# Kernel optimization log

Measured on AMD Instinct MI355X. Metric: run time of the kernel, lower is better.

Reference implementation:

```python
import jax, jax.numpy as jnp
import numpy as np
import math

# ---------- real Clebsch-Gordan coupling tables (computed once, tiny) ----------
def _cg(j1, m1, j2, m2, j3, m3):
    if m1 + m2 != m3 or j3 < abs(j1 - j2) or j3 > j1 + j2:
        return 0.0
    f = math.factorial
    pre = ((2 * j3 + 1) * f(j3 + j1 - j2) * f(j3 - j1 + j2) * f(j1 + j2 - j3) / f(j1 + j2 + j3 + 1)) ** 0.5
    pre *= (f(j3 + m3) * f(j3 - m3) * f(j1 - m1) * f(j1 + m1) * f(j2 - m2) * f(j2 + m2)) ** 0.5
    s = 0.0
    for k in range(0, j1 + j2 - j3 + 1):
        d = (k, j1 + j2 - j3 - k, j1 - m1 - k, j2 + m2 - k, j3 - j2 + m1 + k, j3 - j1 - m2 + k)
        if min(d) < 0:
            continue
        den = 1
        for t in d:
            den *= f(t)
        s += (-1) ** k / den
    return pre * s

def _Q(l):  # complex->real spherical-harmonic change of basis
    Q = np.zeros((2 * l + 1, 2 * l + 1), dtype=complex)
    Q[l, l] = 1.0
    s = 2 ** -0.5
    for m in range(1, l + 1):
        Q[l + m, l + m] = (-1) ** m * s
        Q[l + m, l - m] = s
        Q[l - m, l + m] = -1j * (-1) ** m * s
        Q[l - m, l - m] = 1j * s
    return Q

def _K(l1, l2, l3):  # real coupling tensor [2l3+1, 2l1+1, 2l2+1]
    C = np.zeros((2 * l3 + 1, 2 * l1 + 1, 2 * l2 + 1), dtype=complex)
    for M3 in range(-l3, l3 + 1):
        for M1 in range(-l1, l1 + 1):
            for M2 in range(-l2, l2 + 1):
                C[M3 + l3, M1 + l1, M2 + l2] = _cg(l1, M1, l2, M2, l3, M3)
    K = np.einsum('cC,aA,bB,CAB->cab', _Q(l3).conj(), _Q(l1), _Q(l2), C)
    K = K.imag if np.abs(K.imag).max() > np.abs(K.real).max() else K.real
    return np.asarray(K, dtype=np.float32)

# the 9 'uvu' instructions (in_l, edge_l, out_l) with multiplicities (weight_numel=144)
_PATHS = [(0, 0, 0), (0, 2, 2), (1, 0, 1), (1, 2, 1), (1, 2, 2), (2, 0, 2), (2, 2, 0), (2, 2, 1), (2, 2, 2)]
_KT = [jnp.asarray(_K(*p)) for p in _PATHS]
_MULS = [32, 32, 16, 16, 16, 8, 8, 8, 8]
_SPLITS = np.cumsum(_MULS)[:-1].tolist()
NEI = 8
EPS = 1e-5

def _sh(u):  # component-normalized real SH of unit vectors, l=0..2 (m order -l..l, l=1 -> y,z,x)
    x, y, z = u[:, 0], u[:, 1], u[:, 2]
    sh0 = jnp.ones_like(x)[:, None]
    sh1 = np.float32(3 ** 0.5) * jnp.stack([y, z, x], -1)
    s15 = np.float32(15 ** 0.5)
    s5 = np.float32(5 ** 0.5)
    sh2 = jnp.stack([s15 * x * y, s15 * y * z, 0.5 * s5 * (3 * z * z - 1.0), s15 * x * z, 0.5 * s15 * (x * x - y * y)], -1)
    return sh0, sh1, sh2

def _path(xs, sh, wp, Kt):  # xs [E,u,2l1+1], sh [E,2l2+1], Kt [2l3+1,2l1+1,2l2+1] -> [E,u,2l3+1]
    return jnp.einsum('eui,ej,oij->euo', xs, sh, Kt) * wp[None, :, None]

def _layer(x0, x1, x2, pos, src, dst, w, W0, W1, W2, bw0, bb0, bw1, bw2, N):
    ev = pos[dst] - pos[src]
    u = ev / (jnp.linalg.norm(ev, axis=1, keepdims=True) + 1e-12)
    sh0, sh1, sh2 = _sh(u)
    s0 = x0[src][:, :, None]  # [E,32,1]
    s1 = x1[src]              # [E,16,3]
    s2 = x2[src]              # [E,8,5]
    ws = jnp.split(w, _SPLITS)
    p1 = _path(s0, sh0, ws[0], _KT[0])
    p2 = _path(s0, sh2, ws[1], _KT[1])
    p3 = _path(s1, sh0, ws[2], _KT[2])
    p4 = _path(s1, sh2, ws[3], _KT[3])
    p5 = _path(s1, sh2, ws[4], _KT[4])
    p6 = _path(s2, sh0, ws[5], _KT[5])
    p7 = _path(s2, sh2, ws[6], _KT[6])
    p8 = _path(s2, sh2, ws[7], _KT[7])
    p9 = _path(s2, sh2, ws[8], _KT[8])
    m0 = jnp.concatenate([p1, p7], 1)          # [E,40,1]
    m1 = jnp.concatenate([p3, p4, p8], 1)      # [E,40,3]
    m2 = jnp.concatenate([p2, p5, p6, p9], 1)  # [E,64,5]
    a0 = jax.ops.segment_sum(m0, dst, num_segments=N)
    a1 = jax.ops.segment_sum(m1, dst, num_segments=N)
    a2 = jax.ops.segment_sum(m2, dst, num_segments=N)
    y0 = (a0[:, :, 0] @ W0) * np.float32(1.0 / 40 ** 0.5)
    y1 = jnp.einsum('num,uv->nvm', a1, W1) * np.float32(1.0 / 40 ** 0.5)
    y2 = jnp.einsum('num,uv->nvm', a2, W2) * np.float32(1.0 / 64 ** 0.5)
    # equivariant batchnorm (training stats): scalars -> standard BN, l>0 -> norm BN
    f = y0 - y0.mean(0)
    y0 = f / jnp.sqrt((f * f).mean(0) + EPS) * bw0 + bb0
    y1 = y1 / jnp.sqrt((y1 * y1).mean(axis=(0, 2)) + EPS)[None, :, None] * bw1[None, :, None]
    y2 = y2 / jnp.sqrt((y2 * y2).mean(axis=(0, 2)) + EPS)[None, :, None] * bw2[None, :, None]
    return y0, y1, y2

def _forward(positions, W_emb, tp_w, lin_W0, lin_W1, lin_W2, bn_w0, bn_b0, bn_w1, bn_w2, Wf1, Wf2, bf2, Wf3, bf3):
    B, P, _ = positions.shape
    N = B * P
    pos = positions.reshape(N, 3)
    # kNN graph from dense cdist + topk (indices are not differentiated)
    pg = jax.lax.stop_gradient(pos)
    sq = jnp.sum(pg * pg, 1)
    d2 = sq[:, None] + sq[None, :] - 2.0 * (pg @ pg.T)
    _, idx = jax.lax.top_k(-d2, NEI + 1)  # smallest distances; col 0 is self
    src = jnp.repeat(jnp.arange(N), NEI)
    dst = idx[:, 1:].reshape(-1)
    x0 = jnp.ones((N, 1), jnp.float32) @ W_emb  # embedding: only 0e->0e path exists
    x1 = jnp.zeros((N, 16, 3), jnp.float32)
    x2 = jnp.zeros((N, 8, 5), jnp.float32)
    for l in range(3):
        y0, y1, y2 = _layer(x0, x1, x2, pos, src, dst, tp_w[l], lin_W0[l], lin_W1[l], lin_W2[l],
                            bn_w0[l], bn_b0[l], bn_w1[l], bn_w2[l], N)
        x0 = jax.nn.relu(y0) + x0
        x1 = jax.nn.relu(y1) + x1
        x2 = jax.nn.relu(y2) + x2
    h = jax.nn.relu((x0 @ Wf1) * np.float32(1.0 / 32 ** 0.5))  # scalar part -> 32x0e
    h = jax.nn.relu(h @ Wf2 + bf2)
    out = (h @ Wf3 + bf3).reshape(B, P, 2)
    return out

def setup_inputs() -> dict:
    key = jax.random.key(0)
    ks = jax.random.split(key, 16)
    B, P = 4, 2048
    return {
        'positions': jax.random.normal(ks[0], (B, P, 3), jnp.float32) * 3.0,
        'W_emb': jax.random.normal(ks[1], (1, 32), jnp.float32),
        'tp_w': jax.random.normal(ks[2], (3, 144), jnp.float32),
        'lin_W0': jax.random.normal(ks[3], (3, 40, 32), jnp.float32),
        'lin_W1': jax.random.normal(ks[4], (3, 40, 16), jnp.float32),
        'lin_W2': jax.random.normal(ks[5], (3, 64, 8), jnp.float32),
        'bn_w0': 1.0 + 0.05 * jax.random.normal(ks[6], (3, 32), jnp.float32),
        'bn_b0': jnp.zeros((3, 32), jnp.float32),
        'bn_w1': 1.0 + 0.05 * jax.random.normal(ks[7], (3, 16), jnp.float32),
        'bn_w2': 1.0 + 0.05 * jax.random.normal(ks[8], (3, 8), jnp.float32),
        'Wf1': jax.random.normal(ks[9], (32, 32), jnp.float32),
        'Wf2': jax.random.normal(ks[10], (32, 16), jnp.float32) * 0.2,
        'bf2': jax.random.normal(ks[11], (16,), jnp.float32) * 0.1,
        'Wf3': jax.random.normal(ks[12], (16, 2), jnp.float32) * 0.2,
        'bf3': jax.random.normal(ks[13], (2,), jnp.float32) * 0.1,
    }

def reference(positions, W_emb, tp_w, lin_W0, lin_W1, lin_W2, bn_w0, bn_b0, bn_w1, bn_w2, Wf1, Wf2, bf2, Wf3, bf3):
    return _forward(positions, W_emb, tp_w, lin_W0, lin_W1, lin_W2, bn_w0, bn_b0, bn_w1, bn_w2, Wf1, Wf2, bf2, Wf3, bf3)
```

## Files before the change

kernel.cpp:

```cpp
#include <hip/hip_runtime.h>
#include <math.h>

#define NN 8192
#define REV_CAP 48
#define KNN_CAP 384
#define PF 12

static const size_t OFF_K     = 0;
static const size_t OFF_CNT   = 512;
static const size_t OFF_REV   = 8704;
static const size_t OFF_STATS = 401920;
static const size_t OFF_XF    = 406528;
static const size_t OFF_YF    = 1389568;
static const size_t WS_FLOATS = 2372608;

__device__ double dfact(int n){ double r=1.0; for(int i=2;i<=n;++i) r*=(double)i; return r; }

__device__ double dcg(int j1,int m1,int j2,int m2,int j3,int m3){
  if (m1+m2!=m3) return 0.0;
  if (j3 < abs(j1-j2) || j3 > j1+j2) return 0.0;
  double pre = sqrt((double)(2*j3+1)*dfact(j3+j1-j2)*dfact(j3-j1+j2)*dfact(j1+j2-j3)/dfact(j1+j2+j3+1));
  pre *= sqrt(dfact(j3+m3)*dfact(j3-m3)*dfact(j1-m1)*dfact(j1+m1)*dfact(j2-m2)*dfact(j2+m2));
  double s=0.0;
  for(int k=0;k<=j1+j2-j3;++k){
    int d1=j1+j2-j3-k, d2=j1-m1-k, d3=j2+m2-k, d4=j3-j2+m1+k, d5=j3-j1-m2+k;
    if(d1<0||d2<0||d3<0||d4<0||d5<0) continue;
    double den = dfact(k)*dfact(d1)*dfact(d2)*dfact(d3)*dfact(d4)*dfact(d5);
    s += ((k&1)? -1.0: 1.0)/den;
  }
  return pre*s;
}

__device__ int qrow(int l,int r,int* col,double* re,double* im){
  const double s = 0.70710678118654752440;
  if (r==l){ col[0]=l; re[0]=1.0; im[0]=0.0; return 1; }
  if (r>l){ int m=r-l;
    col[0]=l+m; re[0]=((m&1)?-s:s); im[0]=0.0;
    col[1]=l-m; re[1]=s;            im[1]=0.0;
  } else { int m=l-r;
    col[0]=l+m; re[0]=0.0; im[0]=((m&1)? s : -s);
    col[1]=l-m; re[1]=0.0; im[1]=s;
  }
  return 2;
}

__global__ __launch_bounds__(256) void k_setup(const float* __restrict__ pos,
        const float* __restrict__ W_emb, float* __restrict__ Kbuf,
        float* __restrict__ xf,
        float* __restrict__ xs, float* __restrict__ ys, float* __restrict__ zs,
        float* __restrict__ qs,
        int* __restrict__ cnt){
  int idx = blockIdx.x*256 + threadIdx.x;
  if (idx < 983040) { const int c = idx%120; xf[idx] = (c<32)? W_emb[c] : 0.f; return; }
  idx -= 983040;
  if (idx < 8192) {
    const float x=pos[3*idx], y=pos[3*idx+1], z=pos[3*idx+2];
    xs[idx]=x; ys[idx]=y; zs[idx]=z; qs[idx]=0.5f*(x*x+y*y+z*z);
    return;
  }
  idx -= 8192;
  if (idx < 8192) { cnt[idx]=0; return; }
  idx -= 8192;
  if (idx >= 405) return;

  const int tid = idx;
  const int sizes[9]={1,25,9,45,75,25,25,75,125};
  const int l1s[9]={0,0,1,1,1,2,2,2,2};
  const int l2s[9]={0,2,0,2,2,0,2,2,2};
  const int l3s[9]={0,2,1,1,2,2,0,1,2};
  int p=0, rem=tid;
  for(p=0;p<9;++p){ if(rem < sizes[p]) break; rem -= sizes[p]; }
  const int l1=l1s[p], l2=l2s[p], l3=l3s[p];
  const int n1=2*l1+1, n2=2*l2+1;
  const int c = rem/(n1*n2); const int r2 = rem%(n1*n2); const int a=r2/n2; const int b=r2%n2;

  int c3[2],c1[2],c2[2]; double re3[2],im3[2],re1[2],im1[2],re2[2],im2[2];
  const int nc3 = qrow(l3,c,c3,re3,im3);
  const int nc1 = qrow(l1,a,c1,re1,im1);
  const int nc2 = qrow(l2,b,c2,re2,im2);

  double accRe=0, accIm=0;
  for(int i3=0;i3<nc3;++i3){
    const double q3re=re3[i3], q3im=-im3[i3];
    for(int i1=0;i1<nc1;++i1){
      const double pre_re = q3re*re1[i1] - q3im*im1[i1];
      const double pre_im = q3re*im1[i1] + q3im*re1[i1];
      for(int i2=0;i2<nc2;++i2){
        const double cgv = dcg(l1, c1[i1]-l1, l2, c2[i2]-l2, l3, c3[i3]-l3);
        if (cgv==0.0) continue;
        accRe += (pre_re*re2[i2] - pre_im*im2[i2])*cgv;
        accIm += (pre_re*im2[i2] + pre_im*re2[i2])*cgv;
      }
    }
  }
  const bool useImag = ((l1+l2+l3)&1)!=0;
  Kbuf[tid] = (float)(useImag? accIm : accRe);
}

__device__ __forceinline__ unsigned fkey(float f){
  const unsigned b = __float_as_uint(f);
  return (b & 0x80000000u) ? ~b : (b | 0x80000000u);
}

__global__ __launch_bounds__(256) void k_knn8(const float* __restrict__ xs,
                                              const float* __restrict__ ys,
                                              const float* __restrict__ zs,
                                              const float* __restrict__ qs,
                                              int* __restrict__ cnt, int* __restrict__ rev){
  const int lane = threadIdx.x & 63;
  const int w    = threadIdx.x >> 6;
  const int node = blockIdx.x*4 + w;
  __shared__ float sdist[4][KNN_CAP];
  __shared__ int   sidx[4][KNN_CAP];
  __shared__ int   scount[4];
  if (threadIdx.x < 4) scount[threadIdx.x]=0;
  __syncthreads();

  const float px = xs[node], py = ys[node], pz = zs[node];

  float m1 = INFINITY, m2 = INFINITY;
  for(int c=0;c<4;++c){
    const int base = (c*64 + lane)*4;
    const float4 fx = *(const float4*)(xs + base);
    const float4 fy = *(const float4*)(ys + base);
    const float4 fz = *(const float4*)(zs + base);
    const float4 fq = *(const float4*)(qs + base);
    float ss[4];
    ss[0] = fmaf(-px,fx.x, fmaf(-py,fy.x, fmaf(-pz,fz.x, fq.x)));
    ss[1] = fmaf(-px,fx.y, fmaf(-py,fy.y, fmaf(-pz,fz.y, fq.y)));
    ss[2] = fmaf(-px,fx.z, fmaf(-py,fy.z, fmaf(-pz,fz.z, fq.z)));
    ss[3] = fmaf(-px,fx.w, fmaf(-py,fy.w, fmaf(-pz,fz.w, fq.w)));
    #pragma unroll
    for(int q=0;q<4;++q){
      const float hi = fmaxf(m1, ss[q]);
      m1 = fminf(m1, ss[q]);
      m2 = fminf(m2, hi);
    }
  }
  {
    const unsigned kk1 = fkey(m1), kk2 = fkey(m2);
    unsigned P = 0u; int need = 9;
    #pragma unroll 1
    for(int bit=31; bit>=0; --bit){
      const unsigned pref = P >> bit;
      const int c0 = __popcll(__ballot((kk1>>bit)==pref)) + __popcll(__ballot((kk2>>bit)==pref));
      if (need > c0){ need -= c0; P |= (1u<<bit); }
    }
    m1 = __uint_as_float((P & 0x80000000u) ? (P & 0x7fffffffu) : ~P);
  }
  const float T = m1;

  for(int c=0;c<32;++c){
    const int base = (c*64 + lane)*4;
    const float4 fx = *(const float4*)(xs + base);
    const float4 fy = *(const float4*)(ys + base);
    const float4 fz = *(const float4*)(zs + base);
    const float4 fq = *(const float4*)(qs + base);
    float ss[4];
    ss[0] = fmaf(-px,fx.x, fmaf(-py,fy.x, fmaf(-pz,fz.x, fq.x)));
    ss[1] = fmaf(-px,fx.y, fmaf(-py,fy.y, fmaf(-pz,fz.y, fq.y)));
    ss[2] = fmaf(-px,fx.z, fmaf(-py,fy.z, fmaf(-pz,fz.z, fq.z)));
    ss[3] = fmaf(-px,fx.w, fmaf(-py,fy.w, fmaf(-pz,fz.w, fq.w)));
    #pragma unroll
    for(int q=0;q<4;++q){
      if (ss[q] <= T){
        int pos = atomicAdd(&scount[w],1);
        if (pos < KNN_CAP){ sdist[w][pos]=ss[q]; sidx[w][pos]=base+q; }
      }
    }
  }
  __syncthreads();

  int m = scount[w]; if (m > KNN_CAP) m = KNN_CAP;
  unsigned ku[KNN_CAP/64]; int il[KNN_CAP/64];
  #pragma unroll
  for(int k=0;k<KNN_CAP/64;++k){
    const int j = lane + 64*k;
    if (j < m){ ku[k]=fkey(sdist[w][j]); il[k]=sidx[w][j]; }
    else      { ku[k]=0xffffffffu;       il[k]=0x7fffffff; }
  }
  unsigned P = 0u; int need = 9;
  #pragma unroll 1
  for(int bit=31; bit>=0; --bit){
    const unsigned pref = P >> bit;
    int c0 = 0;
    #pragma unroll
    for(int k=0;k<KNN_CAP/64;++k) c0 += __popcll(__ballot((ku[k]>>bit)==pref));
    if (need > c0){ need -= c0; P |= (1u<<bit); }
  }
  int c_eq = 0;
  #pragma unroll
  for(int k=0;k<KNN_CAP/64;++k) c_eq += __popcll(__ballot(ku[k]==P));
  bool tsel[KNN_CAP/64];
  #pragma unroll
  for(int k=0;k<KNN_CAP/64;++k) tsel[k] = (ku[k]==P);
  if (c_eq > need){
    #pragma unroll
    for(int k=0;k<KNN_CAP/64;++k) tsel[k]=false;
    for(int r=0;r<need;++r){
      int mid = 0x7fffffff;
      #pragma unroll
      for(int k=0;k<KNN_CAP/64;++k) if (ku[k]==P && !tsel[k] && il[k]<mid) mid = il[k];
      #pragma unroll
      for(int s=32;s>0;s>>=1){ const int om = __shfl_xor(mid,s,64); mid = (om<mid)? om : mid; }
      #pragma unroll
      for(int k=0;k<KNN_CAP/64;++k) if (ku[k]==P && il[k]==mid) tsel[k]=true;
    }
  }
  #pragma unroll
  for(int k=0;k<KNN_CAP/64;++k){
    const bool take = (ku[k] < P) || tsel[k];
    const int ix = il[k];
    if (take && ix != node){
      int cpos = atomicAdd(&cnt[ix],1);
      if (cpos < REV_CAP) rev[ix*REV_CAP + cpos] = node;
    }
  }
}

__global__ __launch_bounds__(256) void k_msg(
  const float* __restrict__ pos,
  const int* __restrict__ cnt, const int* __restrict__ rev,
  const float* __restrict__ Kbuf,
  const float* __restrict__ xf,
  const float* __restrict__ tpw,
  const float* __restrict__ W0, const float* __restrict__ W1, const float* __restrict__ W2,
  float* __restrict__ yf)
{
  const int t = threadIdx.x;
  const int w = t >> 6;
  const int lane = t & 63;
  const int n = blockIdx.x*4 + w;

  __shared__ float KL[405];
  __shared__ float TW[144];
  __shared__ float momP[4][120];
  __shared__ float momS[4][600];
  __shared__ float aS[4][480];
  __shared__ int   eIdx[4][REV_CAP];
  __shared__ float eSh[4][5][REV_CAP];
  for(int q=t;q<405;q+=256) KL[q]=Kbuf[q];
  for(int q=t;q<144;q+=256) TW[q]=tpw[q];

  const int deg0 = cnt[n];
  const int deg = (deg0<REV_CAP)? deg0 : REV_CAP;
  const float pnx=pos[3*n], pny=pos[3*n+1], pnz=pos[3*n+2];
  const float s15 = 3.8729833462f, s5c = 2.2360679775f;
  if (lane < deg){
    const int i = rev[n*REV_CAP+lane];
    eIdx[w][lane] = i;
    const float ex = pnx - pos[3*i], ey = pny - pos[3*i+1], ez = pnz - pos[3*i+2];
    const float rn = sqrtf(ex*ex+ey*ey+ez*ez) + 1e-12f;
    const float ux=ex/rn, uy=ey/rn, uz=ez/rn;
    eSh[w][0][lane]=s15*ux*uy;
    eSh[w][1][lane]=s15*uy*uz;
    eSh[w][2][lane]=0.5f*s5c*(3.f*uz*uz-1.f);
    eSh[w][3][lane]=s15*ux*uz;
    eSh[w][4][lane]=0.5f*s15*(ux*ux-uy*uy);
  }
  __syncthreads();

  const int c0 = lane*2;
  float mp0=0.f, mp1=0.f;
  float ms0[5], ms1[5];
  #pragma unroll
  for(int j=0;j<5;++j){ ms0[j]=0.f; ms1[j]=0.f; }

  int idxr[PF];
  #pragma unroll
  for(int k=0;k<PF;++k) idxr[k] = (k<deg)? eIdx[w][k] : 0;
  float2 fr[PF];
  if (lane<60){
    #pragma unroll
    for(int k=0;k<PF;++k) fr[k] = *(const float2*)(xf + (size_t)idxr[k]*120 + c0);
  }
  #pragma unroll
  for(int k=0;k<PF;++k){
    if (k<deg){
      const float sh0=eSh[w][0][k], sh1=eSh[w][1][k], sh2=eSh[w][2][k];
      const float sh3=eSh[w][3][k], sh4=eSh[w][4][k];
      if (lane<60){
        const float2 f = fr[k];
        mp0 += f.x; mp1 += f.y;
        ms0[0]+=f.x*sh0; ms0[1]+=f.x*sh1; ms0[2]+=f.x*sh2; ms0[3]+=f.x*sh3; ms0[4]+=f.x*sh4;
        ms1[0]+=f.y*sh0; ms1[1]+=f.y*sh1; ms1[2]+=f.y*sh2; ms1[3]+=f.y*sh3; ms1[4]+=f.y*sh4;
      }
    }
  }
  for(int e=PF;e<deg;++e){
    const int i = eIdx[w][e];
    const float sh0=eSh[w][0][e], sh1=eSh[w][1][e], sh2=eSh[w][2][e];
    const float sh3=eSh[w][3][e], sh4=eSh[w][4][e];
    if (lane<60){
      const float2 f = *(const float2*)(xf + (size_t)i*120 + c0);
      mp0 += f.x; mp1 += f.y;
      ms0[0]+=f.x*sh0; ms0[1]+=f.x*sh1; ms0[2]+=f.x*sh2; ms0[3]+=f.x*sh3; ms0[4]+=f.x*sh4;
      ms1[0]+=f.y*sh0; ms1[1]+=f.y*sh1; ms1[2]+=f.y*sh2; ms1[3]+=f.y*sh3; ms1[4]+=f.y*sh4;
    }
  }
  if (lane<60){
    momP[w][c0]=mp0; momP[w][c0+1]=mp1;
    #pragma unroll
    for(int j=0;j<5;++j){ momS[w][c0*5+j]=ms0[j]; momS[w][(c0+1)*5+j]=ms1[j]; }
  }
  __syncthreads();

  float acc[14];
  #pragma unroll
  for(int k=0;k<14;++k) acc[k]=0.f;

  if (lane<32){
    const int u=lane;
    const float rw0=TW[u], rw1=TW[32+u];
    acc[0] = rw0 * KL[0] * momP[w][u];
    float m0s[5];
    #pragma unroll
    for(int j=0;j<5;++j) m0s[j]=momS[w][u*5+j];
    #pragma unroll
    for(int o=0;o<5;++o){ float g=0.f;
      #pragma unroll
      for(int j=0;j<5;++j) g += KL[1+o*5+j]*m0s[j];
      acc[1+o] = rw1*g; }
  } else if (lane<48){
    const int u=lane-32;
    const float rw0=TW[64+u], rw1=TW[80+u], rw2=TW[96+u];
    float m1p[3], m1s[3][5];
    #pragma unroll
    for(int i=0;i<3;++i){
      m1p[i]=momP[w][32+u*3+i];
      #pragma unroll
      for(int j=0;j<5;++j) m1s[i][j]=momS[w][(32+u*3+i)*5+j];
    }
    #pragma unroll
    for(int o=0;o<3;++o){ float g=0.f;
      #pragma unroll
      for(int i=0;i<3;++i) g += KL[26+o*3+i]*m1p[i];
      acc[o]=rw0*g; }
    #pragma unroll
    for(int o=0;o<3;++o){ float g=0.f;
      #pragma unroll
      for(int i=0;i<3;++i)
        #pragma unroll
        for(int j=0;j<5;++j) g += KL[35+(o*3+i)*5+j]*m1s[i][j];
      acc[3+o]=rw1*g; }
    #pragma unroll
    for(int o=0;o<5;++o){ float g=0.f;
      #pragma unroll
      for(int i=0;i<3;++i)
        #pragma unroll
        for(int j=0;j<5;++j) g += KL[80+(o*3+i)*5+j]*m1s[i][j];
      acc[6+o]=rw2*g; }
  } else if (lane<56){
    const int u=lane-48;
    const float rw0=TW[112+u], rw1=TW[120+u], rw2=TW[128+u], rw3=TW[136+u];
    float m2p[5], m2s[5][5];
    #pragma unroll
    for(int i=0;i<5;++i){
      m2p[i]=momP[w][80+u*5+i];
      #pragma unroll
      for(int j=0;j<5;++j) m2s[i][j]=momS[w][(80+u*5+i)*5+j];
    }
    #pragma unroll
    for(int o=0;o<5;++o){ float g=0.f;
      #pragma unroll
      for(int i=0;i<5;++i) g += KL[155+o*5+i]*m2p[i];
      acc[o]=rw0*g; }
    { float g=0.f;
      #pragma unroll
      for(int i=0;i<5;++i)
        #pragma unroll
        for(int j=0;j<5;++j) g += KL[180+i*5+j]*m2s[i][j];
      acc[5]=rw1*g; }
    #pragma unroll
    for(int o=0;o<3;++o){ float g=0.f;
      #pragma unroll
      for(int i=0;i<5;++i)
        #pragma unroll
        for(int j=0;j<5;++j) g += KL[205+(o*5+i)*5+j]*m2s[i][j];
      acc[6+o]=rw2*g; }
    #pragma unroll
    for(int o=0;o<5;++o){ float g=0.f;
      #pragma unroll
      for(int i=0;i<5;++i)
        #pragma unroll
        for(int j=0;j<5;++j) g += KL[280+(o*5+i)*5+j]*m2s[i][j];
      acc[9+o]=rw3*g; }
  }

  if (lane<32){
    aS[w][lane] = acc[0];
    #pragma unroll
    for(int o=0;o<5;++o) aS[w][160 + lane*5+o] = acc[1+o];
  } else if (lane<48){
    const int uu=lane-32;
    #pragma unroll
    for(int m=0;m<3;++m){ aS[w][40 + uu*3+m] = acc[m]; aS[w][40 + (16+uu)*3+m] = acc[3+m]; }
    #pragma unroll
    for(int o=0;o<5;++o) aS[w][160 + (32+uu)*5+o] = acc[6+o];
  } else if (lane<56){
    const int uu=lane-48;
    aS[w][32+uu] = acc[5];
    #pragma unroll
    for(int m=0;m<3;++m) aS[w][40 + (32+uu)*3+m] = acc[6+m];
    #pragma unroll
    for(int o=0;o<5;++o){ aS[w][160 + (48+uu)*5+o] = acc[o]; aS[w][160 + (56+uu)*5+o] = acc[9+o]; }
  }
  __syncthreads();

  const float inv40 = 0.15811388300841896660f;
  for(int q=lane;q<120;q+=64){
    float out;
    if (q<32){
      float g=0.f;
      for(int uu=0;uu<40;++uu) g += aS[w][uu]*W0[uu*32+q];
      out = g*inv40;
    } else if (q<80){
      const int e=q-32, v=e/3, m=e%3;
      float g=0.f;
      for(int uu=0;uu<40;++uu) g += aS[w][40+uu*3+m]*W1[uu*16+v];
      out = g*inv40;
    } else {
      const int e=q-80, tt=e/5, m=e%5;
      float g=0.f;
      for(int uu=0;uu<64;++uu) g += aS[w][160+uu*5+m]*W2[uu*8+tt];
      out = g*0.125f;
    }
    yf[(size_t)n*120+q] = out;
  }
}

__global__ __launch_bounds__(256) void k_statp(const float* __restrict__ yf,
                                               float* __restrict__ pA, float* __restrict__ pB){
  const int ch = blockIdx.x % 96;
  const int chunk = blockIdx.x / 96;
  const int t = threadIdx.x;
  const int n0 = chunk*1024;
  __shared__ float r1[256], r2[256];
  float a1=0.f, a2=0.f;
  if (ch<32){
    for(int nn=t;nn<1024;nn+=256){ float v=yf[(size_t)(n0+nn)*120+ch]; a1+=v; a2+=v*v; }
  } else if (ch<48){
    const int v_=ch-32;
    for(int nn=t;nn<1024;nn+=256){
      #pragma unroll
      for(int m=0;m<3;++m){ float v=yf[(size_t)(n0+nn)*120+32+v_*3+m]; a2+=v*v; }
    }
  } else {
    const int t_=ch-48;
    for(int nn=t;nn<1024;nn+=256){
      #pragma unroll
      for(int m=0;m<5;++m){ float v=yf[(size_t)(n0+nn)*120+80+t_*5+m]; a2+=v*v; }
    }
  }
  r1[t]=a1; r2[t]=a2; __syncthreads();
  for(int s=128;s>0;s>>=1){ if(t<s){ r1[t]+=r1[t+s]; r2[t]+=r2[t+s]; } __syncthreads(); }
  if(t==0){ pA[ch*8+chunk]=r1[0]; pB[ch*8+chunk]=r2[0]; }
}

__global__ __launch_bounds__(256) void k_norm(const float* __restrict__ yf,
                       const float* __restrict__ pA, const float* __restrict__ pB,
                       const float* __restrict__ bw0,const float* __restrict__ bb0,
                       const float* __restrict__ bw1,const float* __restrict__ bw2,
                       float* __restrict__ xf){
  __shared__ float sc[96], sf[32];
  const int t = threadIdx.x;
  if (t<96){
    float sB=0.f;
    #pragma unroll
    for(int k=0;k<8;++k) sB += pB[t*8+k];
    float scale;
    if (t<32){
      float sA=0.f;
      #pragma unroll
      for(int k=0;k<8;++k) sA += pA[t*8+k];
      const float mean = sA*(1.f/8192.f);
      const float var  = sB*(1.f/8192.f) - mean*mean;
      const float inv  = 1.f/sqrtf(var+1e-5f);
      scale = bw0[t]*inv;
      sf[t] = bb0[t] - mean*scale;
    } else if (t<48){
      scale = bw1[t-32]/sqrtf(sB*(1.f/(8192.f*3.f))+1e-5f);
    } else {
      scale = bw2[t-48]/sqrtf(sB*(1.f/(8192.f*5.f))+1e-5f);
    }
    sc[t]=scale;
  }
  __syncthreads();
  const int idx = blockIdx.x*256 + t;
  if (idx >= NN*120) return;
  const int c = idx%120;
  const int chan = (c<32)? c : ((c<80)? 32+(c-32)/3 : 48+(c-80)/5);
  const float v = yf[idx]*sc[chan] + ((c<32)? sf[c] : 0.f);
  xf[idx] += fmaxf(v,0.f);
}

__global__ __launch_bounds__(256) void k_normmlp(const float* __restrict__ yf,
                                             const float* __restrict__ xf,
                                             const float* __restrict__ pA, const float* __restrict__ pB,
                                             const float* __restrict__ bw0,const float* __restrict__ bb0,
                                             const float* __restrict__ Wf1,const float* __restrict__ Wf2,
                                             const float* __restrict__ bf2,const float* __restrict__ Wf3,
                                             const float* __restrict__ bf3, float* __restrict__ out){
  __shared__ float w1[1024], w2[512], w3[32], b2[16], b3[2], sc0[32], sf0[32];
  const int t=threadIdx.x;
  for(int q=t;q<1024;q+=256) w1[q]=Wf1[q];
  for(int q=t;q<512;q+=256)  w2[q]=Wf2[q];
  if(t<32) w3[t]=Wf3[t];
  if(t<16) b2[t]=bf2[t];
  if(t<2)  b3[t]=bf3[t];
  if(t<32){
    float sA=0.f, sB=0.f;
    #pragma unroll
    for(int k=0;k<8;++k){ sA += pA[t*8+k]; sB += pB[t*8+k]; }
    const float mean = sA*(1.f/8192.f);
    const float var  = sB*(1.f/8192.f) - mean*mean;
    const float inv  = 1.f/sqrtf(var+1e-5f);
    sc0[t] = bw0[t]*inv;
    sf0[t] = bb0[t] - mean*sc0[t];
  }
  __syncthreads();
  const int n = blockIdx.x*256+t;
  if(n>=NN) return;
  float xv[32];
  #pragma unroll
  for(int k=0;k<32;++k){
    const float v = yf[(size_t)n*120+k]*sc0[k] + sf0[k];
    xv[k] = xf[(size_t)n*120+k] + fmaxf(v,0.f);
  }
  const float inv32 = 0.17677669529663688110f;
  float h1[32];
  #pragma unroll 4
  for(int c=0;c<32;++c){ float g=0.f;
    #pragma unroll
    for(int k=0;k<32;++k) g+=xv[k]*w1[k*32+c];
    h1[c]=fmaxf(g*inv32,0.f); }
  float h2[16];
  #pragma unroll 4
  for(int c=0;c<16;++c){ float g=b2[c];
    #pragma unroll
    for(int k=0;k<32;++k) g+=h1[k]*w2[k*16+c];
    h2[c]=fmaxf(g,0.f); }
  #pragma unroll
  for(int m=0;m<2;++m){ float g=b3[m];
    #pragma unroll
    for(int k=0;k<16;++k) g+=h2[k]*w3[k*2+m];
    out[n*2+m]=g; }
}

extern "C" void kernel_launch(void* const* d_in, const int* in_sizes, int n_in,
                              void* d_out, int out_size, void* d_ws, size_t ws_size,
                              hipStream_t stream) {
  const float* positions = (const float*)d_in[0];
  const float* W_emb  = (const float*)d_in[1];
  const float* tp_w   = (const float*)d_in[2];
  const float* lin_W0 = (const float*)d_in[3];
  const float* lin_W1 = (const float*)d_in[4];
  const float* lin_W2 = (const float*)d_in[5];
  const float* bn_w0  = (const float*)d_in[6];
  const float* bn_b0  = (const float*)d_in[7];
  const float* bn_w1  = (const float*)d_in[8];
  const float* bn_w2  = (const float*)d_in[9];
  const float* Wf1 = (const float*)d_in[10];
  const float* Wf2 = (const float*)d_in[11];
  const float* bf2 = (const float*)d_in[12];
  const float* Wf3 = (const float*)d_in[13];
  const float* bf3 = (const float*)d_in[14];

  if (ws_size < WS_FLOATS*sizeof(float)) return;

  float* ws    = (float*)d_ws;
  float* Kbuf  = ws + OFF_K;
  int*   cnt   = (int*)(ws + OFF_CNT);
  int*   rev   = (int*)(ws + OFF_REV);
  float* stats = ws + OFF_STATS;
  float* xf = ws + OFF_XF;
  float* yf = ws + OFF_YF;

  float* xs = yf;
  float* ysA = yf + NN;
  float* zs = yf + 2*NN;
  float* qs = yf + 3*NN;

  k_setup<<<3906,256,0,stream>>>(positions, W_emb, Kbuf, xf, xs, ysA, zs, qs, cnt);
  k_knn8<<<NN/4,256,0,stream>>>(xs, ysA, zs, qs, cnt, rev);

  for(int l=0;l<3;++l){
    float* pA = stats + l*1536;
    float* pB = pA + 768;
    k_msg<<<NN/4,256,0,stream>>>(positions, cnt, rev, Kbuf, xf,
                              tp_w + l*144, lin_W0 + l*40*32, lin_W1 + l*40*16, lin_W2 + l*64*8,
                              yf);
    k_statp<<<768,256,0,stream>>>(yf, pA, pB);
    if (l<2){
      k_norm<<<(NN*120+255)/256,256,0,stream>>>(yf, pA, pB,
                              bn_w0 + l*32, bn_b0 + l*32, bn_w1 + l*16, bn_w2 + l*8,
                              xf);
    }
  }
  k_normmlp<<<NN/256,256,0,stream>>>(yf, xf, stats + 2*1536, stats + 2*1536 + 768,
                              bn_w0 + 64, bn_b0 + 64,
                              Wf1, Wf2, bf2, Wf3, bf3, (float*)d_out);
}
```

Before: 293.6 us.

## Fuse batch-norm statistics into message kernel and trim kNN selection

The per-channel sum and sum-of-squares reduction moves from a separate k_statp pass into the tail of k_msg. It uses shared-memory atomics per block, then global atomics into 8 slots per channel that are zeroed in k_setup. This removes three launches and three rereads of yf. The kNN kernel also gets register prefetching of the next candidate chunk, an occupancy hint in launch_bounds, and a smaller radix select when there are at most 128 candidates. Float atomics make the statistic summation order nondeterministic.

```diff
diff --git a/kernel.cpp b/kernel.cpp
--- a/kernel.cpp
+++ b/kernel.cpp
@@ -49,7 +49,7 @@
         float* __restrict__ xf,
         float* __restrict__ xs, float* __restrict__ ys, float* __restrict__ zs,
         float* __restrict__ qs,
-        int* __restrict__ cnt){
+        int* __restrict__ cnt, float* __restrict__ stats){
   int idx = blockIdx.x*256 + threadIdx.x;
   if (idx < 983040) { const int c = idx%120; xf[idx] = (c<32)? W_emb[c] : 0.f; return; }
   idx -= 983040;
@@ -61,6 +61,8 @@
   idx -= 8192;
   if (idx < 8192) { cnt[idx]=0; return; }
   idx -= 8192;
+  if (idx < 4608) { stats[idx]=0.f; return; }
+  idx -= 4608;
   if (idx >= 405) return;
 
   const int tid = idx;
@@ -102,7 +104,47 @@
   return (b & 0x80000000u) ? ~b : (b | 0x80000000u);
 }
 
-__global__ __launch_bounds__(256) void k_knn8(const float* __restrict__ xs,
+#define RSELECT_PUSH(KMAX) do{ \
+  unsigned P = 0u; int need = 9; \
+  _Pragma("unroll 1") \
+  for(int bit=31; bit>=0; --bit){ \
+    const unsigned pref = P >> bit; \
+    int c0 = 0; \
+    _Pragma("unroll") \
+    for(int k=0;k<KMAX;++k) c0 += __popcll(__ballot((ku[k]>>bit)==pref)); \
+    if (need > c0){ need -= c0; P |= (1u<<bit); } \
+  } \
+  int c_eq = 0; \
+  _Pragma("unroll") \
+  for(int k=0;k<KMAX;++k) c_eq += __popcll(__ballot(ku[k]==P)); \
+  bool tsel[KMAX]; \
+  _Pragma("unroll") \
+  for(int k=0;k<KMAX;++k) tsel[k] = (ku[k]==P); \
+  if (c_eq > need){ \
+    _Pragma("unroll") \
+    for(int k=0;k<KMAX;++k) tsel[k]=false; \
+    for(int r=0;r<need;++r){ \
+      int mid = 0x7fffffff; \
+      _Pragma("unroll") \
+      for(int k=0;k<KMAX;++k) if (ku[k]==P && !tsel[k] && il[k]<mid) mid = il[k]; \
+      _Pragma("unroll") \
+      for(int s=32;s>0;s>>=1){ const int om = __shfl_xor(mid,s,64); mid = (om<mid)? om : mid; } \
+      _Pragma("unroll") \
+      for(int k=0;k<KMAX;++k) if (ku[k]==P && il[k]==mid) tsel[k]=true; \
+    } \
+  } \
+  _Pragma("unroll") \
+  for(int k=0;k<KMAX;++k){ \
+    const bool take = (ku[k] < P) || tsel[k]; \
+    const int ix = il[k]; \
+    if (take && ix != node){ \
+      int cpos = atomicAdd(&cnt[ix],1); \
+      if (cpos < REV_CAP) rev[ix*REV_CAP + cpos] = node; \
+    } \
+  } \
+}while(0)
+
+__global__ __launch_bounds__(256, 8) void k_knn8(const float* __restrict__ xs,
                                               const float* __restrict__ ys,
                                               const float* __restrict__ zs,
                                               const float* __restrict__ qs,
@@ -150,22 +192,33 @@
   }
   const float T = m1;
 
-  for(int c=0;c<32;++c){
-    const int base = (c*64 + lane)*4;
-    const float4 fx = *(const float4*)(xs + base);
-    const float4 fy = *(const float4*)(ys + base);
-    const float4 fz = *(const float4*)(zs + base);
-    const float4 fq = *(const float4*)(qs + base);
-    float ss[4];
-    ss[0] = fmaf(-px,fx.x, fmaf(-py,fy.x, fmaf(-pz,fz.x, fq.x)));
-    ss[1] = fmaf(-px,fx.y, fmaf(-py,fy.y, fmaf(-pz,fz.y, fq.y)));
-    ss[2] = fmaf(-px,fx.z, fmaf(-py,fy.z, fmaf(-pz,fz.z, fq.z)));
-    ss[3] = fmaf(-px,fx.w, fmaf(-py,fy.w, fmaf(-pz,fz.w, fq.w)));
-    #pragma unroll
-    for(int q=0;q<4;++q){
-      if (ss[q] <= T){
-        int pos = atomicAdd(&scount[w],1);
-        if (pos < KNN_CAP){ sdist[w][pos]=ss[q]; sidx[w][pos]=base+q; }
+  {
+    const int b0 = lane*4;
+    float4 nfx = *(const float4*)(xs + b0);
+    float4 nfy = *(const float4*)(ys + b0);
+    float4 nfz = *(const float4*)(zs + b0);
+    float4 nfq = *(const float4*)(qs + b0);
+    for(int c=0;c<32;++c){
+      const float4 fx=nfx, fy=nfy, fz=nfz, fq=nfq;
+      const int cbase = (c*64 + lane)*4;
+      if (c<31){
+        const int nb2 = ((c+1)*64 + lane)*4;
+        nfx = *(const float4*)(xs + nb2);
+        nfy = *(const float4*)(ys + nb2);
+        nfz = *(const float4*)(zs + nb2);
+        nfq = *(const float4*)(qs + nb2);
+      }
+      float ss[4];
+      ss[0] = fmaf(-px,fx.x, fmaf(-py,fy.x, fmaf(-pz,fz.x, fq.x)));
+      ss[1] = fmaf(-px,fx.y, fmaf(-py,fy.y, fmaf(-pz,fz.y, fq.y)));
+      ss[2] = fmaf(-px,fx.z, fmaf(-py,fy.z, fmaf(-pz,fz.z, fq.z)));
+      ss[3] = fmaf(-px,fx.w, fmaf(-py,fy.w, fmaf(-pz,fz.w, fq.w)));
+      #pragma unroll
+      for(int q=0;q<4;++q){
+        if (ss[q] <= T){
+          int pos = atomicAdd(&scount[w],1);
+          if (pos < KNN_CAP){ sdist[w][pos]=ss[q]; sidx[w][pos]=cbase+q; }
+        }
       }
     }
   }
@@ -179,43 +232,8 @@
     if (j < m){ ku[k]=fkey(sdist[w][j]); il[k]=sidx[w][j]; }
     else      { ku[k]=0xffffffffu;       il[k]=0x7fffffff; }
   }
-  unsigned P = 0u; int need = 9;
-  #pragma unroll 1
-  for(int bit=31; bit>=0; --bit){
-    const unsigned pref = P >> bit;
-    int c0 = 0;
-    #pragma unroll
-    for(int k=0;k<KNN_CAP/64;++k) c0 += __popcll(__ballot((ku[k]>>bit)==pref));
-    if (need > c0){ need -= c0; P |= (1u<<bit); }
-  }
-  int c_eq = 0;
-  #pragma unroll
-  for(int k=0;k<KNN_CAP/64;++k) c_eq += __popcll(__ballot(ku[k]==P));
-  bool tsel[KNN_CAP/64];
-  #pragma unroll
-  for(int k=0;k<KNN_CAP/64;++k) tsel[k] = (ku[k]==P);
-  if (c_eq > need){
-    #pragma unroll
-    for(int k=0;k<KNN_CAP/64;++k) tsel[k]=false;
-    for(int r=0;r<need;++r){
-      int mid = 0x7fffffff;
-      #pragma unroll
-      for(int k=0;k<KNN_CAP/64;++k) if (ku[k]==P && !tsel[k] && il[k]<mid) mid = il[k];
-      #pragma unroll
-      for(int s=32;s>0;s>>=1){ const int om = __shfl_xor(mid,s,64); mid = (om<mid)? om : mid; }
-      #pragma unroll
-      for(int k=0;k<KNN_CAP/64;++k) if (ku[k]==P && il[k]==mid) tsel[k]=true;
-    }
-  }
-  #pragma unroll
-  for(int k=0;k<KNN_CAP/64;++k){
-    const bool take = (ku[k] < P) || tsel[k];
-    const int ix = il[k];
-    if (take && ix != node){
-      int cpos = atomicAdd(&cnt[ix],1);
-      if (cpos < REV_CAP) rev[ix*REV_CAP + cpos] = node;
-    }
-  }
+  if (m <= 128) RSELECT_PUSH(2);
+  else          RSELECT_PUSH(6);
 }
 
 __global__ __launch_bounds__(256) void k_msg(
@@ -225,6 +243,7 @@
   const float* __restrict__ xf,
   const float* __restrict__ tpw,
   const float* __restrict__ W0, const float* __restrict__ W1, const float* __restrict__ W2,
+  float* __restrict__ pA, float* __restrict__ pB,
   float* __restrict__ yf)
 {
   const int t = threadIdx.x;
@@ -239,8 +258,10 @@
   __shared__ float aS[4][480];
   __shared__ int   eIdx[4][REV_CAP];
   __shared__ float eSh[4][5][REV_CAP];
+  __shared__ float bA[32], bB[96];
   for(int q=t;q<405;q+=256) KL[q]=Kbuf[q];
   for(int q=t;q<144;q+=256) TW[q]=tpw[q];
+  if (t<96){ bB[t]=0.f; if(t<32) bA[t]=0.f; }
 
   const int deg0 = cnt[n];
   const int deg = (deg0<REV_CAP)? deg0 : REV_CAP;
@@ -409,52 +430,32 @@
 
   const float inv40 = 0.15811388300841896660f;
   for(int q=lane;q<120;q+=64){
-    float out;
+    float out; int chan;
     if (q<32){
       float g=0.f;
       for(int uu=0;uu<40;++uu) g += aS[w][uu]*W0[uu*32+q];
-      out = g*inv40;
+      out = g*inv40; chan = q;
     } else if (q<80){
       const int e=q-32, v=e/3, m=e%3;
       float g=0.f;
       for(int uu=0;uu<40;++uu) g += aS[w][40+uu*3+m]*W1[uu*16+v];
-      out = g*inv40;
+      out = g*inv40; chan = 32+v;
     } else {
       const int e=q-80, tt=e/5, m=e%5;
       float g=0.f;
       for(int uu=0;uu<64;++uu) g += aS[w][160+uu*5+m]*W2[uu*8+tt];
-      out = g*0.125f;
+      out = g*0.125f; chan = 48+tt;
     }
     yf[(size_t)n*120+q] = out;
-  }
-}
-
-__global__ __launch_bounds__(256) void k_statp(const float* __restrict__ yf,
-                                               float* __restrict__ pA, float* __restrict__ pB){
-  const int ch = blockIdx.x % 96;
-  const int chunk = blockIdx.x / 96;
-  const int t = threadIdx.x;
-  const int n0 = chunk*1024;
-  __shared__ float r1[256], r2[256];
-  float a1=0.f, a2=0.f;
-  if (ch<32){
-    for(int nn=t;nn<1024;nn+=256){ float v=yf[(size_t)(n0+nn)*120+ch]; a1+=v; a2+=v*v; }
-  } else if (ch<48){
-    const int v_=ch-32;
-    for(int nn=t;nn<1024;nn+=256){
-      #pragma unroll
-      for(int m=0;m<3;++m){ float v=yf[(size_t)(n0+nn)*120+32+v_*3+m]; a2+=v*v; }
-    }
-  } else {
-    const int t_=ch-48;
-    for(int nn=t;nn<1024;nn+=256){
-      #pragma unroll
-      for(int m=0;m<5;++m){ float v=yf[(size_t)(n0+nn)*120+80+t_*5+m]; a2+=v*v; }
-    }
-  }
-  r1[t]=a1; r2[t]=a2; __syncthreads();
-  for(int s=128;s>0;s>>=1){ if(t<s){ r1[t]+=r1[t+s]; r2[t]+=r2[t+s]; } __syncthreads(); }
-  if(t==0){ pA[ch*8+chunk]=r1[0]; pB[ch*8+chunk]=r2[0]; }
+    atomicAdd(&bB[chan], out*out);
+    if (q<32) atomicAdd(&bA[q], out);
+  }
+  __syncthreads();
+  if (t<96){
+    const int slot = blockIdx.x & 7;
+    atomicAdd(&pB[t*8 + slot], bB[t]);
+    if (t<32) atomicAdd(&pA[t*8 + slot], bA[t]);
+  }
 }
 
 __global__ __launch_bounds__(256) void k_norm(const float* __restrict__ yf,
@@ -581,7 +582,7 @@
   float* zs = yf + 2*NN;
   float* qs = yf + 3*NN;
 
-  k_setup<<<3906,256,0,stream>>>(positions, W_emb, Kbuf, xf, xs, ysA, zs, qs, cnt);
+  k_setup<<<3924,256,0,stream>>>(positions, W_emb, Kbuf, xf, xs, ysA, zs, qs, cnt, stats);
   k_knn8<<<NN/4,256,0,stream>>>(xs, ysA, zs, qs, cnt, rev);
 
   for(int l=0;l<3;++l){
@@ -589,8 +590,7 @@
     float* pB = pA + 768;
     k_msg<<<NN/4,256,0,stream>>>(positions, cnt, rev, Kbuf, xf,
                               tp_w + l*144, lin_W0 + l*40*32, lin_W1 + l*40*16, lin_W2 + l*64*8,
-                              yf);
-    k_statp<<<768,256,0,stream>>>(yf, pA, pB);
+                              pA, pB, yf);
     if (l<2){
       k_norm<<<(NN*120+255)/256,256,0,stream>>>(yf, pA, pB,
                               bn_w0 + l*32, bn_b0 + l*32, bn_w1 + l*16, bn_w2 + l*8,
```

After: 365.0 us. +24.3%, slower.
